# Optimization experiments

Measured on AMD Instinct MI355X. Metric: run time of the kernel, lower is better.

The kernel has to match this reference:

```python
import math
import jax, jax.numpy as jnp
import numpy as np

# ---- model dims ----
D = 4096          # hidden_size
N = 32            # num_attention_heads (== num_key_value_heads)
Q_LORA = 1536
KV_LORA = 512
QK_NOPE = 128
QK_ROPE = 64
QK_HEAD = QK_NOPE + QK_ROPE   # 192
V_HEAD = 128
EPS = 1e-6
T = 2048

# ---- yarn rope constants ----
ROPE_THETA = 10000.0
FACTOR = 40.0
ORIG_MAX = 4096
BETA_FAST = 32.0
BETA_SLOW = 1.0
MSCALE = 1.0
MSCALE_ALL_DIM = 1.0


def _yarn_get_mscale(scale, mscale):
    if scale <= 1.0:
        return 1.0
    return 0.1 * mscale * math.log(scale) + 1.0

# softmax scale: qk_head_dim^-0.5 * yarn_mscale^2 (rope_mscale_all_dim = 1.0)
YARN_MSCALE = _yarn_get_mscale(FACTOR, MSCALE_ALL_DIM)
SM_SCALE = QK_HEAD ** (-0.5) * YARN_MSCALE ** 2


def _yarn_cos_sin(positions):
    """DeepSeek yarn scaled rotary embeddings. positions: int [T]."""
    half = QK_ROPE // 2
    pow_ = np.arange(0, QK_ROPE, 2, dtype=np.float64) / QK_ROPE
    pos_freqs = ROPE_THETA ** pow_
    inv_extra = 1.0 / pos_freqs
    inv_inter = 1.0 / (FACTOR * pos_freqs)

    def corr_dim(n_rot):
        return (QK_ROPE * math.log(ORIG_MAX / (n_rot * 2 * math.pi))) / (2 * math.log(ROPE_THETA))

    low = max(math.floor(corr_dim(BETA_FAST)), 0)
    high = min(math.ceil(corr_dim(BETA_SLOW)), QK_ROPE - 1)
    ramp = np.clip((np.arange(half, dtype=np.float64) - low) / max(high - low, 1e-3), 0.0, 1.0)
    mask = 1.0 - ramp  # 1 where extrapolation
    inv_freq = inv_inter * (1.0 - mask) + inv_extra * mask
    inv_freq = jnp.asarray(inv_freq, jnp.float32)

    mscale_coef = _yarn_get_mscale(FACTOR, MSCALE) / _yarn_get_mscale(FACTOR, MSCALE_ALL_DIM)
    t = positions.astype(jnp.float32)
    freqs = t[:, None] * inv_freq[None, :]          # [T, half]
    return jnp.cos(freqs) * mscale_coef, jnp.sin(freqs) * mscale_coef


def _apply_rope(x_tnh, cos, sin):
    """Neox-style (split halves) rope. x: [T, N, QK_ROPE]; cos/sin: [T, half]."""
    half = QK_ROPE // 2
    x1, x2 = x_tnh[..., :half], x_tnh[..., half:]
    c, s = cos[:, None, :], sin[:, None, :]
    return jnp.concatenate([x1 * c - x2 * s, x1 * s + x2 * c], axis=-1)


def _rms_norm(x, scale, eps=EPS):
    var = jnp.mean(jnp.square(x), axis=-1, keepdims=True)
    return x * jax.lax.rsqrt(var + eps) * scale


def setup_inputs() -> dict:
    key = jax.random.key(0)
    ks = jax.random.split(key, 8)
    std = 0.02
    return {
        "x": jax.random.normal(ks[0], (T, D), jnp.float32),
        "positions": jnp.arange(T, dtype=jnp.int32),
        "w_q_down": jax.random.normal(ks[1], (D, Q_LORA), jnp.float32) * std,
        "q_norm_scale": jnp.ones((Q_LORA,), jnp.float32),
        "w_q_up": jax.random.normal(ks[2], (Q_LORA, N, QK_HEAD), jnp.float32) * std,
        "w_kv_down": jax.random.normal(ks[3], (D, KV_LORA + QK_ROPE), jnp.float32) * std,
        "kv_norm_scale": jnp.ones((KV_LORA,), jnp.float32),
        "w_kv_up": jax.random.normal(ks[4], (KV_LORA, N, QK_NOPE + V_HEAD), jnp.float32) * std,
        "w_o": jax.random.normal(ks[5], (N, V_HEAD, D), jnp.float32) * std,
    }


def reference(x, positions, w_q_down, q_norm_scale, w_q_up, w_kv_down,
              kv_norm_scale, w_kv_up, w_o):
    cos, sin = _yarn_cos_sin(positions)

    # ---- q projection (low rank) ----
    q_ta = _rms_norm(jnp.einsum('td,da->ta', x, w_q_down), q_norm_scale)
    q_tnh = jnp.einsum('ta,anh->tnh', q_ta, w_q_up)            # [T,N,192]
    q_rope = _apply_rope(q_tnh[..., QK_NOPE:], cos, sin)
    q_tnh = jnp.concatenate([q_tnh[..., :QK_NOPE], q_rope], axis=-1)

    # ---- kv projection (compressed latent) ----
    kv_sa = jnp.einsum('sd,da->sa', x, w_kv_down)              # [T, KV_LORA+64]
    k_rope = _apply_rope(kv_sa[:, None, KV_LORA:], cos, sin)   # [T,1,64]
    k_rope = jnp.broadcast_to(k_rope, (x.shape[0], N, QK_ROPE))
    kv_lat = _rms_norm(kv_sa[..., :KV_LORA], kv_norm_scale)
    kv_nope = jnp.einsum('sa,anh->snh', kv_lat, w_kv_up)       # [T,N,256]
    k_snh = jnp.concatenate([kv_nope[..., :QK_NOPE], k_rope], axis=-1)
    v_snh = kv_nope[..., QK_NOPE:]

    # ---- causal attention (prefill; padding to 128-multiple is a no-op) ----
    scores = jnp.einsum('tnh,snh->nts', q_tnh, k_snh) * SM_SCALE
    tpos = jnp.arange(x.shape[0])
    causal = tpos[:, None] >= tpos[None, :]
    scores = jnp.where(causal[None, :, :], scores, jnp.finfo(scores.dtype).min)
    probs = jax.nn.softmax(scores, axis=-1)
    out_tnh = jnp.einsum('nts,snh->tnh', probs, v_snh)

    # ---- output projection ----
    return jnp.einsum('tnh,nhd->td', out_tnh, w_o)
```

## Files before the change

### kernel.cpp

```cpp
#include <hip/hip_runtime.h>
#include <math.h>
#include <stdint.h>

#define T_    2048
#define D_    4096
#define NH_   32
#define QL_   1536
#define KVL_  512
#define ROPE_ 64
#define NOPE_ 128
#define HQK_  192
#define HV_   128
#define KVD_  576
#define NCAT_ 2112

typedef __bf16 bf16x8 __attribute__((ext_vector_type(8)));
typedef __bf16 bf16x4 __attribute__((ext_vector_type(4)));
typedef float f32x4 __attribute__((ext_vector_type(4)));

__device__ __forceinline__ void gload_lds16(const __bf16* g, __bf16* l) {
  __builtin_amdgcn_global_load_lds(
      (const __attribute__((address_space(1))) void*)g,
      (__attribute__((address_space(3))) void*)l, 16, 0, 0);
}

template <typename OutT>
__global__ __launch_bounds__(256, 3) void mfma_gemm_kernel(
    const __bf16* __restrict__ A, const __bf16* __restrict__ Bt,
    OutT* __restrict__ C, int M, int Ncols, int K) {
  __shared__ __bf16 As[128 * 64];
  __shared__ __bf16 Bs[128 * 64];
  const int tid = threadIdx.x;
  const int lane = tid & 63;
  const int w = tid >> 6;
  const int wm = w >> 1, wn = w & 1;
  const int lg = lane >> 4, lj = lane & 15;
  const int bm = blockIdx.y * 128;
  const int bn = blockIdx.x * 128;

  const __bf16* ga[4]; const __bf16* gb[4];
  int ldsoff[4];
  #pragma unroll
  for (int i = 0; i < 4; ++i) {
    int task = i * 256 + tid;
    int r = task >> 3, cl = task & 7;
    int cg = cl ^ (r & 7);
    ga[i] = A  + (size_t)(bm + r) * K + cg * 8;
    gb[i] = Bt + (size_t)(bn + r) * K + cg * 8;
    ldsoff[i] = (i * 256 + w * 64) * 8;
  }

  f32x4 acc[4][4];
  #pragma unroll
  for (int mi = 0; mi < 4; ++mi)
    #pragma unroll
    for (int ni = 0; ni < 4; ++ni) acc[mi][ni] = (f32x4){0.f, 0.f, 0.f, 0.f};

  for (int k0 = 0; k0 < K; k0 += 64) {
    __syncthreads();
    #pragma unroll
    for (int i = 0; i < 4; ++i) gload_lds16(ga[i] + k0, &As[ldsoff[i]]);
    #pragma unroll
    for (int i = 0; i < 4; ++i) gload_lds16(gb[i] + k0, &Bs[ldsoff[i]]);
    __syncthreads();
    #pragma unroll
    for (int kh = 0; kh < 2; ++kh) {
      bf16x8 af[4], bfr[4];
      #pragma unroll
      for (int i = 0; i < 4; ++i) {
        int ra = wm * 64 + i * 16 + lj;
        af[i] = *(const bf16x8*)&As[ra * 64 + ((((kh << 2) + lg) ^ (ra & 7)) << 3)];
      }
      #pragma unroll
      for (int i = 0; i < 4; ++i) {
        int rb = wn * 64 + i * 16 + lj;
        bfr[i] = *(const bf16x8*)&Bs[rb * 64 + ((((kh << 2) + lg) ^ (rb & 7)) << 3)];
      }
      #pragma unroll
      for (int mi = 0; mi < 4; ++mi)
        #pragma unroll
        for (int ni = 0; ni < 4; ++ni)
          acc[mi][ni] = __builtin_amdgcn_mfma_f32_16x16x32_bf16(af[mi], bfr[ni], acc[mi][ni], 0, 0, 0);
    }
  }

  #pragma unroll
  for (int mi = 0; mi < 4; ++mi) {
    #pragma unroll
    for (int r = 0; r < 4; ++r) {
      int row = bm + wm * 64 + mi * 16 + lg * 4 + r;
      #pragma unroll
      for (int ni = 0; ni < 4; ++ni) {
        int col = bn + wn * 64 + ni * 16 + lj;
        if (col < Ncols) C[(size_t)row * Ncols + col] = (OutT)acc[mi][ni][r];
      }
    }
  }
}

__global__ __launch_bounds__(256) void transpose_bf16_kernel(
    const float* __restrict__ B, __bf16* __restrict__ Bt, int K, int N) {
  __shared__ float tile[64][65];
  int n0 = blockIdx.x * 64, k0 = blockIdx.y * 64;
  int tid = threadIdx.x;
  int kr = tid >> 4, nc = (tid & 15) * 4;
  #pragma unroll
  for (int i = 0; i < 4; ++i) {
    int k = kr + i * 16;
    float4 v = make_float4(0.f, 0.f, 0.f, 0.f);
    if (n0 + nc < N) v = *(const float4*)(B + (size_t)(k0 + k) * N + n0 + nc);
    tile[k][nc + 0] = v.x; tile[k][nc + 1] = v.y;
    tile[k][nc + 2] = v.z; tile[k][nc + 3] = v.w;
  }
  __syncthreads();
  int nl = tid >> 4, k4 = (tid & 15) * 4;
  #pragma unroll
  for (int i = 0; i < 4; ++i) {
    int nn = nl + i * 16;
    bf16x4 o;
    o[0] = (__bf16)tile[k4 + 0][nn]; o[1] = (__bf16)tile[k4 + 1][nn];
    o[2] = (__bf16)tile[k4 + 2][nn]; o[3] = (__bf16)tile[k4 + 3][nn];
    *(bf16x4*)(Bt + (size_t)(n0 + nn) * K + k0 + k4) = o;
  }
}

__global__ __launch_bounds__(256) void conv_bf16_kernel(
    const float* __restrict__ in, __bf16* __restrict__ out, int n8) {
  int i = blockIdx.x * 256 + threadIdx.x;
  if (i >= n8) return;
  float4 a = *(const float4*)(in + (size_t)i * 8);
  float4 b = *(const float4*)(in + (size_t)i * 8 + 4);
  bf16x8 v;
  v[0] = (__bf16)a.x; v[1] = (__bf16)a.y; v[2] = (__bf16)a.z; v[3] = (__bf16)a.w;
  v[4] = (__bf16)b.x; v[5] = (__bf16)b.y; v[6] = (__bf16)b.z; v[7] = (__bf16)b.w;
  *(bf16x8*)(out + (size_t)i * 8) = v;
}

__global__ __launch_bounds__(256) void rmsnorm_bf16_kernel(
    const __bf16* __restrict__ in, __bf16* __restrict__ out,
    const float* __restrict__ scale, int len, int in_stride) {
  int row = blockIdx.x;
  const __bf16* x = in + (size_t)row * in_stride;
  __bf16* y = out + (size_t)row * len;
  float ss = 0.f;
  for (int i = threadIdx.x; i < len; i += 256) { float v = (float)x[i]; ss += v * v; }
  __shared__ float red[4];
  #pragma unroll
  for (int o = 32; o > 0; o >>= 1) ss += __shfl_down(ss, o, 64);
  int wid = threadIdx.x >> 6, lane = threadIdx.x & 63;
  if (lane == 0) red[wid] = ss;
  __syncthreads();
  if (threadIdx.x == 0) {
    float t = red[0] + red[1] + red[2] + red[3];
    red[0] = 1.0f / sqrtf(t / (float)len + 1e-6f);
  }
  __syncthreads();
  float r = red[0];
  for (int i = threadIdx.x; i < len; i += 256) y[i] = (__bf16)((float)x[i] * r * scale[i]);
}

struct InvFreq { float f[32]; };
__global__ __launch_bounds__(256) void rope_table_kernel(
    const int* __restrict__ pos, float* __restrict__ cosT, float* __restrict__ sinT,
    InvFreq invf) {
  int idx = blockIdx.x * 256 + threadIdx.x;
  if (idx >= T_ * 32) return;
  int t = idx >> 5, i = idx & 31;
  float fr = (float)pos[t] * invf.f[i];
  cosT[idx] = cosf(fr);
  sinT[idx] = sinf(fr);
}

__global__ __launch_bounds__(256) void rope_q_kernel(
    __bf16* __restrict__ q, const float* __restrict__ cosT, const float* __restrict__ sinT) {
  int idx = blockIdx.x * 256 + threadIdx.x;
  if (idx >= T_ * NH_ * 32) return;
  int i = idx & 31;
  int tn = idx >> 5;
  int t = tn >> 5;
  __bf16* b = q + (size_t)tn * HQK_ + NOPE_;
  float x1 = (float)b[i], x2 = (float)b[i + 32];
  float c = cosT[t * 32 + i], s = sinT[t * 32 + i];
  b[i]      = (__bf16)(x1 * c - x2 * s);
  b[i + 32] = (__bf16)(x1 * s + x2 * c);
}

__global__ __launch_bounds__(256) void rope_k_kernel(
    const __bf16* __restrict__ src, int stride, const float* __restrict__ cosT,
    const float* __restrict__ sinT, __bf16* __restrict__ k_rope) {
  int idx = blockIdx.x * 256 + threadIdx.x;
  if (idx >= T_ * 32) return;
  int t = idx >> 5, i = idx & 31;
  const __bf16* b = src + (size_t)t * stride;
  float x1 = (float)b[i], x2 = (float)b[i + 32];
  float c = cosT[idx], s = sinT[idx];
  k_rope[t * 64 + i]      = (__bf16)(x1 * c - x2 * s);
  k_rope[t * 64 + i + 32] = (__bf16)(x1 * s + x2 * c);
}

__global__ __launch_bounds__(256) void prep_vt_kernel(
    const __bf16* __restrict__ kv_nopeb, __bf16* __restrict__ Vt) {
  __shared__ __bf16 tile[64][136];
  int s0 = blockIdx.x * 64;
  int n = blockIdx.y;
  int tid = threadIdx.x;
  #pragma unroll
  for (int i = 0; i < 4; ++i) {
    int idx = tid + i * 256;
    int s = idx >> 4, c = idx & 15;
    bf16x8 v = *(const bf16x8*)(kv_nopeb + ((size_t)(s0 + s) * NH_ + n) * 256 + NOPE_ + c * 8);
    *(bf16x8*)&tile[s][c * 8] = v;
  }
  __syncthreads();
  #pragma unroll
  for (int i = 0; i < 8; ++i) {
    int idx = tid + i * 256;
    int h = idx >> 4, s4 = (idx & 15) * 4;
    bf16x4 v;
    v[0] = tile[s4 + 0][h]; v[1] = tile[s4 + 1][h];
    v[2] = tile[s4 + 2][h]; v[3] = tile[s4 + 3][h];
    *(bf16x4*)(Vt + ((size_t)n * HV_ + h) * T_ + s0 + s4) = v;
  }
}

__global__ __launch_bounds__(256, 2) void attn_mfma_kernel(
    const __bf16* __restrict__ q_tnh, const __bf16* __restrict__ kv_nopeb,
    const __bf16* __restrict__ k_rope, const __bf16* __restrict__ Vt,
    __bf16* __restrict__ attn_out, float sm_scale2) {
  __shared__ __bf16 KsL[2][24 * 64 * 8];
  __shared__ __bf16 Vs[8 * 128 * 8];
  __shared__ __bf16 Ps[4][32 * 64];
  const int tid = threadIdx.x;
  const int lane = tid & 63;
  const int w = tid >> 6;
  const int id = blockIdx.x;
  const int j = id >> 3;
  const int p = j >> 2;
  const int n = (id & 7) * 4 + (j & 3);
  const int lg = lane >> 4;
  const int lj = lane & 15;
  const int qtf0 = p, qtf1 = 31 - p;

  const __bf16* kptr[6]; size_t kstep[6]; int klds[6];
  #pragma unroll
  for (int i = 0; i < 6; ++i) {
    int task = i * 256 + tid;
    int c = task >> 6, s = task & 63;
    if (c < 16) { kptr[i] = kv_nopeb + ((size_t)s * NH_ + n) * 256 + c * 8; kstep[i] = (size_t)64 * NH_ * 256; }
    else        { kptr[i] = k_rope + (size_t)s * ROPE_ + (c - 16) * 8;      kstep[i] = (size_t)64 * ROPE_; }
    klds[i] = (i * 256 + w * 64) * 8;
  }
  const __bf16* vptr[4]; int vlds[4];
  #pragma unroll
  for (int i = 0; i < 4; ++i) {
    int task = i * 256 + tid;
    int c = task >> 7, h = task & 127;
    vptr[i] = Vt + ((size_t)n * HV_ + h) * T_ + c * 8;
    vlds[i] = (i * 256 + w * 64) * 8;
  }

  #define STAGE_K(bufIdx)                                                      \
    do {                                                                       \
      __bf16* kb_ = &KsL[bufIdx][0];                                           \
      _Pragma("unroll")                                                        \
      for (int i_ = 0; i_ < 6; ++i_) {                                         \
        gload_lds16(kptr[i_], kb_ + klds[i_]);                                 \
        kptr[i_] += kstep[i_];                                                 \
      }                                                                        \
    } while (0)
  #define STAGE_V()                                                            \
    do {                                                                       \
      _Pragma("unroll")                                                        \
      for (int i_ = 0; i_ < 4; ++i_) {                                         \
        gload_lds16(vptr[i_], &Vs[0] + vlds[i_]);                              \
        vptr[i_] += 64;                                                        \
      }                                                                        \
    } while (0)

  STAGE_K(0);

  bf16x8 qf[2][6];
  #pragma unroll
  for (int f = 0; f < 2; ++f) {
    int t = (f ? qtf1 : qtf0) * 64 + w * 16 + lj;
    const __bf16* qp = q_tnh + ((size_t)t * NH_ + n) * HQK_;
    #pragma unroll
    for (int kk = 0; kk < 6; ++kk) {
      bf16x8 raw = *(const bf16x8*)(qp + kk * 32 + lg * 8);
      bf16x8 v;
      #pragma unroll
      for (int i = 0; i < 8; ++i) v[i] = (__bf16)((float)raw[i] * sm_scale2);
      qf[f][kk] = v;
    }
  }

  f32x4 O[2][8];
  float m_r[2][4], l_r[2][4];
  #pragma unroll
  for (int f = 0; f < 2; ++f) {
    #pragma unroll
    for (int nb = 0; nb < 8; ++nb) O[f][nb] = (f32x4){0.f, 0.f, 0.f, 0.f};
    #pragma unroll
    for (int r = 0; r < 4; ++r) { m_r[f][r] = -1e30f; l_r[f][r] = 0.f; }
  }

  __syncthreads();

  const int nst = 32 - p;
  #pragma unroll 1
  for (int st = 0; st < nst; ++st) {
    const int s0 = st * 64;
    const int cur = st & 1;
    if (st + 1 < nst) STAGE_K(cur ^ 1);
    STAGE_V();
    const __bf16* kb = &KsL[cur][0];
    const bool act0 = (st <= qtf0);

    #pragma unroll
    for (int f = 0; f < 2; ++f) {
      if (f == 0 && !act0) continue;
      const int qt = f ? qtf1 : qtf0;
      const int rowbase = qt * 64 + w * 16;
      f32x4 S[4];
      __builtin_amdgcn_s_setprio(1);
      #pragma unroll
      for (int sb = 0; sb < 4; ++sb) {
        f32x4 acc = (f32x4){0.f, 0.f, 0.f, 0.f};
        int srow = sb * 16 + lj;
        #pragma unroll
        for (int kk = 0; kk < 6; ++kk) {
          int c = kk * 4 + lg;
          bf16x8 b = *(const bf16x8*)&kb[(c * 64 + srow) * 8];
          acc = __builtin_amdgcn_mfma_f32_16x16x32_bf16(qf[f][kk], b, acc, 0, 0, 0);
        }
        S[sb] = acc;
      }
      __builtin_amdgcn_s_setprio(0);
      if (st == qt) {
        #pragma unroll
        for (int sb = 0; sb < 4; ++sb)
          #pragma unroll
          for (int r = 0; r < 4; ++r) {
            int row = rowbase + lg * 4 + r;
            int col = s0 + sb * 16 + lj;
            if (col > row) S[sb][r] = -1e30f;
          }
      }
      float mx[4];
      #pragma unroll
      for (int r = 0; r < 4; ++r) {
        float m2 = fmaxf(fmaxf(S[0][r], S[1][r]), fmaxf(S[2][r], S[3][r]));
        m2 = fmaxf(m2, __shfl_xor(m2, 1));
        m2 = fmaxf(m2, __shfl_xor(m2, 2));
        m2 = fmaxf(m2, __shfl_xor(m2, 4));
        m2 = fmaxf(m2, __shfl_xor(m2, 8));
        mx[r] = m2;
      }
      int need = (mx[0] > m_r[f][0]) | (mx[1] > m_r[f][1]) |
                 (mx[2] > m_r[f][2]) | (mx[3] > m_r[f][3]);
      if (__any(need)) {
        #pragma unroll
        for (int r = 0; r < 4; ++r) {
          float mnew = fmaxf(m_r[f][r], mx[r]);
          float corr = __builtin_amdgcn_exp2f(m_r[f][r] - mnew);
          m_r[f][r] = mnew;
          l_r[f][r] *= corr;
          #pragma unroll
          for (int nb = 0; nb < 8; ++nb) O[f][nb][r] = O[f][nb][r] * corr;
        }
      }
      #pragma unroll
      for (int r = 0; r < 4; ++r) {
        float psum = 0.f;
        #pragma unroll
        for (int sb = 0; sb < 4; ++sb) {
          float pp = __builtin_amdgcn_exp2f(S[sb][r] - m_r[f][r]);
          S[sb][r] = pp;
          psum += pp;
        }
        l_r[f][r] += psum;
      }
      #pragma unroll
      for (int sb = 0; sb < 4; ++sb) {
        int sl = sb * 16 + lj;
        int c = sl >> 3;
        #pragma unroll
        for (int r = 0; r < 4; ++r) {
          int rw = lg * 4 + r;
          Ps[w][(f * 16 + rw) * 64 + ((c ^ (rw & 7)) << 3) + (sl & 7)] = (__bf16)S[sb][r];
        }
      }
    }
    __syncthreads();
    __builtin_amdgcn_s_setprio(1);
    #pragma unroll
    for (int f = 0; f < 2; ++f) {
      if (f == 0 && !act0) continue;
      #pragma unroll
      for (int kk = 0; kk < 2; ++kk) {
        int ca = kk * 4 + lg;
        bf16x8 pa = *(const bf16x8*)&Ps[w][(f * 16 + lj) * 64 + ((ca ^ (lj & 7)) << 3)];
        #pragma unroll
        for (int nb = 0; nb < 8; ++nb) {
          int h = nb * 16 + lj;
          bf16x8 bv = *(const bf16x8*)&Vs[(ca * 128 + h) * 8];
          O[f][nb] = __builtin_amdgcn_mfma_f32_16x16x32_bf16(pa, bv, O[f][nb], 0, 0, 0);
        }
      }
    }
    __builtin_amdgcn_s_setprio(0);
    __syncthreads();
  }

  #pragma unroll
  for (int f = 0; f < 2; ++f) {
    const int qt = f ? qtf1 : qtf0;
    #pragma unroll
    for (int r = 0; r < 4; ++r) {
      float lsum = l_r[f][r];
      lsum += __shfl_xor(lsum, 1);
      lsum += __shfl_xor(lsum, 2);
      lsum += __shfl_xor(lsum, 4);
      lsum += __shfl_xor(lsum, 8);
      float inv = 1.0f / lsum;
      int t = qt * 64 + w * 16 + lg * 4 + r;
      __bf16* dst = attn_out + ((size_t)t * NH_ + n) * HV_;
      #pragma unroll
      for (int nb = 0; nb < 8; ++nb) dst[nb * 16 + lj] = (__bf16)(O[f][nb][r] * inv);
    }
  }
  #undef STAGE_K
  #undef STAGE_V
}

static void compute_inv_freq(float* out) {
  const double theta = 10000.0, factor = 40.0;
  const double PI = 3.14159265358979323846;
  const int rot = ROPE_;
  double low_d  = rot * log(4096.0 / (32.0 * 2.0 * PI)) / (2.0 * log(theta));
  double high_d = rot * log(4096.0 / ( 1.0 * 2.0 * PI)) / (2.0 * log(theta));
  double low = floor(low_d);  if (low < 0) low = 0;
  double high = ceil(high_d); if (high > rot - 1) high = rot - 1;
  for (int i = 0; i < 32; ++i) {
    double pf = pow(theta, (2.0 * i) / (double)rot);
    double inv_extra = 1.0 / pf;
    double inv_inter = 1.0 / (factor * pf);
    double ramp = ((double)i - low) / fmax(high - low, 0.001);
    ramp = fmin(fmax(ramp, 0.0), 1.0);
    double mask = 1.0 - ramp;
    out[i] = (float)(inv_inter * (1.0 - mask) + inv_extra * mask);
  }
}

extern "C" void kernel_launch(void* const* d_in, const int* in_sizes, int n_in,
                              void* d_out, int out_size, void* d_ws, size_t ws_size,
                              hipStream_t stream) {
  const float* x            = (const float*)d_in[0];
  const int*   positions    = (const int*)d_in[1];
  const float* w_q_down     = (const float*)d_in[2];
  const float* q_norm_scale = (const float*)d_in[3];
  const float* w_q_up       = (const float*)d_in[4];
  const float* w_kv_down    = (const float*)d_in[5];
  const float* kv_norm_scale= (const float*)d_in[6];
  const float* w_kv_up      = (const float*)d_in[7];
  const float* w_o          = (const float*)d_in[8];
  float* out = (float*)d_out;

  float* ws = (float*)d_ws;
  float*  cosT     = ws;
  float*  sinT     = ws + 65536;
  __bf16* catb     = (__bf16*)(ws + 131072);
  __bf16* xb       = (__bf16*)(ws + 4456448);
  __bf16* Bt_cat   = (__bf16*)(ws + 8650752);
  __bf16* Bt_qu    = (__bf16*)(ws + 13107200);
  __bf16* Bt_kvu   = (__bf16*)(ws + 17825792);
  __bf16* q_tab    = (__bf16*)(ws + 19922944);
  __bf16* kv_latb  = (__bf16*)(ws + 21495808);
  __bf16* k_ropeb  = (__bf16*)(ws + 22020096);
  __bf16* q_tnhb   = (__bf16*)(ws + 22085632);
  __bf16* kv_nopeb = (__bf16*)(ws + 28377088);
  __bf16* Vt       = (__bf16*)(ws + 13107200);
  __bf16* attn_ob  = (__bf16*)(ws + 17825792);
  __bf16* Bt_o     = (__bf16*)(ws + 4456448);
  (void)ws_size; (void)n_in; (void)in_sizes; (void)out_size;

  InvFreq invf;
  compute_inv_freq(invf.f);
  double ym = 0.1 * log(40.0) + 1.0;
  float sm_scale2 = (float)((ym * ym / sqrt((double)HQK_)) * 1.44269504088896340736);

  rope_table_kernel<<<(T_ * 32 + 255) / 256, 256, 0, stream>>>(positions, cosT, sinT, invf);
  conv_bf16_kernel<<<T_ * D_ / 8 / 256, 256, 0, stream>>>(x, xb, T_ * D_ / 8);
  transpose_bf16_kernel<<<dim3(QL_ / 64, D_ / 64), 256, 0, stream>>>(w_q_down, Bt_cat, D_, QL_);
  transpose_bf16_kernel<<<dim3(KVD_ / 64, D_ / 64), 256, 0, stream>>>(w_kv_down, Bt_cat + (size_t)QL_ * D_, D_, KVD_);
  transpose_bf16_kernel<<<dim3(NH_ * HQK_ / 64, QL_ / 64), 256, 0, stream>>>(w_q_up, Bt_qu, QL_, NH_ * HQK_);
  transpose_bf16_kernel<<<dim3(NH_ * 256 / 64, KVL_ / 64), 256, 0, stream>>>(w_kv_up, Bt_kvu, KVL_, NH_ * 256);

  mfma_gemm_kernel<__bf16><<<dim3((NCAT_ + 127) / 128, T_ / 128), 256, 0, stream>>>(xb, Bt_cat, catb, T_, NCAT_, D_);

  rmsnorm_bf16_kernel<<<T_, 256, 0, stream>>>(catb, q_tab, q_norm_scale, QL_, NCAT_);
  mfma_gemm_kernel<__bf16><<<dim3(NH_ * HQK_ / 128, T_ / 128), 256, 0, stream>>>(q_tab, Bt_qu, q_tnhb, T_, NH_ * HQK_, QL_);
  rope_q_kernel<<<(T_ * NH_ * 32 + 255) / 256, 256, 0, stream>>>(q_tnhb, cosT, sinT);

  rmsnorm_bf16_kernel<<<T_, 256, 0, stream>>>(catb + QL_, kv_latb, kv_norm_scale, KVL_, NCAT_);
  rope_k_kernel<<<(T_ * 32 + 255) / 256, 256, 0, stream>>>(catb + QL_ + KVL_, NCAT_, cosT, sinT, k_ropeb);
  mfma_gemm_kernel<__bf16><<<dim3(NH_ * 256 / 128, T_ / 128), 256, 0, stream>>>(kv_latb, Bt_kvu, kv_nopeb, T_, NH_ * 256, KVL_);

  prep_vt_kernel<<<dim3(T_ / 64, NH_), 256, 0, stream>>>(kv_nopeb, Vt);
  attn_mfma_kernel<<<512, 256, 0, stream>>>(q_tnhb, kv_nopeb, k_ropeb, Vt, attn_ob, sm_scale2);

  transpose_bf16_kernel<<<dim3(D_ / 64, NH_ * HV_ / 64), 256, 0, stream>>>(w_o, Bt_o, NH_ * HV_, D_);
  mfma_gemm_kernel<float><<<dim3(D_ / 128, T_ / 128), 256, 0, stream>>>(attn_ob, Bt_o, out, T_, D_, NH_ * HV_);
}
```

Baseline: 412.3 us.

## Fuse V transpose into kv-up GEMM epilogue and use BK=128 for down projection

The kv-up projection GEMM now computes the V half of each head with operands swapped, so it writes V already transposed into the Vt buffer. This removes the separate prep_vt transpose kernel and its extra read and write of V. The fused down projection uses a new GEMM variant with a 128-wide K tile, halving the number of K iterations and barriers, at the cost of 64KB of LDS per block. The transposed stores are less coalesced than the normal epilogue.

```diff
diff --git a/kernel.cpp b/kernel.cpp
--- a/kernel.cpp
+++ b/kernel.cpp
@@ -98,6 +98,179 @@
   }
 }
 
+template <typename OutT>
+__global__ __launch_bounds__(256, 2) void mfma_gemm_bk128_kernel(
+    const __bf16* __restrict__ A, const __bf16* __restrict__ Bt,
+    OutT* __restrict__ C, int M, int Ncols, int K) {
+  __shared__ __bf16 As[128 * 128];
+  __shared__ __bf16 Bs[128 * 128];
+  const int tid = threadIdx.x;
+  const int lane = tid & 63;
+  const int w = tid >> 6;
+  const int wm = w >> 1, wn = w & 1;
+  const int lg = lane >> 4, lj = lane & 15;
+  const int bm = blockIdx.y * 128;
+  const int bn = blockIdx.x * 128;
+
+  const __bf16* ga[8]; const __bf16* gb[8];
+  int ldsoff[8];
+  #pragma unroll
+  for (int i = 0; i < 8; ++i) {
+    int task = i * 256 + tid;
+    int r = task >> 4, cl = task & 15;
+    int cg = (cl & 8) | ((cl & 7) ^ (r & 7));
+    ga[i] = A  + (size_t)(bm + r) * K + cg * 8;
+    gb[i] = Bt + (size_t)(bn + r) * K + cg * 8;
+    ldsoff[i] = (i * 256 + w * 64) * 8;
+  }
+
+  f32x4 acc[4][4];
+  #pragma unroll
+  for (int mi = 0; mi < 4; ++mi)
+    #pragma unroll
+    for (int ni = 0; ni < 4; ++ni) acc[mi][ni] = (f32x4){0.f, 0.f, 0.f, 0.f};
+
+  for (int k0 = 0; k0 < K; k0 += 128) {
+    __syncthreads();
+    #pragma unroll
+    for (int i = 0; i < 8; ++i) gload_lds16(ga[i] + k0, &As[ldsoff[i]]);
+    #pragma unroll
+    for (int i = 0; i < 8; ++i) gload_lds16(gb[i] + k0, &Bs[ldsoff[i]]);
+    __syncthreads();
+    #pragma unroll
+    for (int kh = 0; kh < 4; ++kh) {
+      bf16x8 af[4], bfr[4];
+      #pragma unroll
+      for (int i = 0; i < 4; ++i) {
+        int ra = wm * 64 + i * 16 + lj;
+        int kc = (kh << 2) + lg;
+        int slot = (kc & 8) | ((kc & 7) ^ (ra & 7));
+        af[i] = *(const bf16x8*)&As[ra * 128 + (slot << 3)];
+      }
+      #pragma unroll
+      for (int i = 0; i < 4; ++i) {
+        int rb = wn * 64 + i * 16 + lj;
+        int kc = (kh << 2) + lg;
+        int slot = (kc & 8) | ((kc & 7) ^ (rb & 7));
+        bfr[i] = *(const bf16x8*)&Bs[rb * 128 + (slot << 3)];
+      }
+      #pragma unroll
+      for (int mi = 0; mi < 4; ++mi)
+        #pragma unroll
+        for (int ni = 0; ni < 4; ++ni)
+          acc[mi][ni] = __builtin_amdgcn_mfma_f32_16x16x32_bf16(af[mi], bfr[ni], acc[mi][ni], 0, 0, 0);
+    }
+  }
+
+  #pragma unroll
+  for (int mi = 0; mi < 4; ++mi) {
+    #pragma unroll
+    for (int r = 0; r < 4; ++r) {
+      int row = bm + wm * 64 + mi * 16 + lg * 4 + r;
+      #pragma unroll
+      for (int ni = 0; ni < 4; ++ni) {
+        int col = bn + wn * 64 + ni * 16 + lj;
+        if (col < Ncols) C[(size_t)row * Ncols + col] = (OutT)acc[mi][ni][r];
+      }
+    }
+  }
+}
+
+__global__ __launch_bounds__(256, 3) void kvup_gemm_kernel(
+    const __bf16* __restrict__ A ,
+    const __bf16* __restrict__ Bt ,
+    __bf16* __restrict__ kv_nopeb ,
+    __bf16* __restrict__ Vt ) {
+  __shared__ __bf16 As[128 * 64];
+  __shared__ __bf16 Bs[128 * 64];
+  const int tid = threadIdx.x;
+  const int lane = tid & 63;
+  const int w = tid >> 6;
+  const int wm = w >> 1, wn = w & 1;
+  const int lg = lane >> 4, lj = lane & 15;
+  const int bm = blockIdx.y * 128;
+  const int bn = blockIdx.x * 128;
+  const int n = blockIdx.x >> 1;
+  const bool vhalf = (blockIdx.x & 1) != 0;
+  const int K = KVL_;
+
+  const __bf16* ga[4]; const __bf16* gb[4];
+  int ldsoff[4];
+  #pragma unroll
+  for (int i = 0; i < 4; ++i) {
+    int task = i * 256 + tid;
+    int r = task >> 3, cl = task & 7;
+    int cg = cl ^ (r & 7);
+    ga[i] = A  + (size_t)(bm + r) * K + cg * 8;
+    gb[i] = Bt + (size_t)(bn + r) * K + cg * 8;
+    ldsoff[i] = (i * 256 + w * 64) * 8;
+  }
+
+  const __bf16* RowT = vhalf ? &Bs[0] : &As[0];
+  const __bf16* ColT = vhalf ? &As[0] : &Bs[0];
+
+  f32x4 acc[4][4];
+  #pragma unroll
+  for (int mi = 0; mi < 4; ++mi)
+    #pragma unroll
+    for (int ni = 0; ni < 4; ++ni) acc[mi][ni] = (f32x4){0.f, 0.f, 0.f, 0.f};
+
+  for (int k0 = 0; k0 < K; k0 += 64) {
+    __syncthreads();
+    #pragma unroll
+    for (int i = 0; i < 4; ++i) gload_lds16(ga[i] + k0, &As[ldsoff[i]]);
+    #pragma unroll
+    for (int i = 0; i < 4; ++i) gload_lds16(gb[i] + k0, &Bs[ldsoff[i]]);
+    __syncthreads();
+    #pragma unroll
+    for (int kh = 0; kh < 2; ++kh) {
+      bf16x8 af[4], bfr[4];
+      #pragma unroll
+      for (int i = 0; i < 4; ++i) {
+        int ra = wm * 64 + i * 16 + lj;
+        af[i] = *(const bf16x8*)&RowT[ra * 64 + ((((kh << 2) + lg) ^ (ra & 7)) << 3)];
+      }
+      #pragma unroll
+      for (int i = 0; i < 4; ++i) {
+        int rb = wn * 64 + i * 16 + lj;
+        bfr[i] = *(const bf16x8*)&ColT[rb * 64 + ((((kh << 2) + lg) ^ (rb & 7)) << 3)];
+      }
+      #pragma unroll
+      for (int mi = 0; mi < 4; ++mi)
+        #pragma unroll
+        for (int ni = 0; ni < 4; ++ni)
+          acc[mi][ni] = __builtin_amdgcn_mfma_f32_16x16x32_bf16(af[mi], bfr[ni], acc[mi][ni], 0, 0, 0);
+    }
+  }
+
+  if (!vhalf) {
+    #pragma unroll
+    for (int mi = 0; mi < 4; ++mi)
+      #pragma unroll
+      for (int r = 0; r < 4; ++r) {
+        int s = bm + wm * 64 + mi * 16 + lg * 4 + r;
+        #pragma unroll
+        for (int ni = 0; ni < 4; ++ni) {
+          int c = wn * 64 + ni * 16 + lj;
+          kv_nopeb[((size_t)s * NH_ + n) * 256 + c] = (__bf16)acc[mi][ni][r];
+        }
+      }
+  } else {
+    #pragma unroll
+    for (int mi = 0; mi < 4; ++mi)
+      #pragma unroll
+      for (int r = 0; r < 4; ++r) {
+        int h = wm * 64 + mi * 16 + lg * 4 + r;
+        __bf16* dst = Vt + ((size_t)n * HV_ + h) * T_ + bm;
+        #pragma unroll
+        for (int ni = 0; ni < 4; ++ni) {
+          int s = wn * 64 + ni * 16 + lj;
+          dst[s] = (__bf16)acc[mi][ni][r];
+        }
+      }
+  }
+}
+
 __global__ __launch_bounds__(256) void transpose_bf16_kernel(
     const float* __restrict__ B, __bf16* __restrict__ Bt, int K, int N) {
   __shared__ float tile[64][65];
@@ -196,31 +369,6 @@
   float c = cosT[idx], s = sinT[idx];
   k_rope[t * 64 + i]      = (__bf16)(x1 * c - x2 * s);
   k_rope[t * 64 + i + 32] = (__bf16)(x1 * s + x2 * c);
-}
-
-__global__ __launch_bounds__(256) void prep_vt_kernel(
-    const __bf16* __restrict__ kv_nopeb, __bf16* __restrict__ Vt) {
-  __shared__ __bf16 tile[64][136];
-  int s0 = blockIdx.x * 64;
-  int n = blockIdx.y;
-  int tid = threadIdx.x;
-  #pragma unroll
-  for (int i = 0; i < 4; ++i) {
-    int idx = tid + i * 256;
-    int s = idx >> 4, c = idx & 15;
-    bf16x8 v = *(const bf16x8*)(kv_nopeb + ((size_t)(s0 + s) * NH_ + n) * 256 + NOPE_ + c * 8);
-    *(bf16x8*)&tile[s][c * 8] = v;
-  }
-  __syncthreads();
-  #pragma unroll
-  for (int i = 0; i < 8; ++i) {
-    int idx = tid + i * 256;
-    int h = idx >> 4, s4 = (idx & 15) * 4;
-    bf16x4 v;
-    v[0] = tile[s4 + 0][h]; v[1] = tile[s4 + 1][h];
-    v[2] = tile[s4 + 2][h]; v[3] = tile[s4 + 3][h];
-    *(bf16x4*)(Vt + ((size_t)n * HV_ + h) * T_ + s0 + s4) = v;
-  }
 }
 
 __global__ __launch_bounds__(256, 2) void attn_mfma_kernel(
@@ -496,7 +644,7 @@
   transpose_bf16_kernel<<<dim3(NH_ * HQK_ / 64, QL_ / 64), 256, 0, stream>>>(w_q_up, Bt_qu, QL_, NH_ * HQK_);
   transpose_bf16_kernel<<<dim3(NH_ * 256 / 64, KVL_ / 64), 256, 0, stream>>>(w_kv_up, Bt_kvu, KVL_, NH_ * 256);
 
-  mfma_gemm_kernel<__bf16><<<dim3((NCAT_ + 127) / 128, T_ / 128), 256, 0, stream>>>(xb, Bt_cat, catb, T_, NCAT_, D_);
+  mfma_gemm_bk128_kernel<__bf16><<<dim3((NCAT_ + 127) / 128, T_ / 128), 256, 0, stream>>>(xb, Bt_cat, catb, T_, NCAT_, D_);
 
   rmsnorm_bf16_kernel<<<T_, 256, 0, stream>>>(catb, q_tab, q_norm_scale, QL_, NCAT_);
   mfma_gemm_kernel<__bf16><<<dim3(NH_ * HQK_ / 128, T_ / 128), 256, 0, stream>>>(q_tab, Bt_qu, q_tnhb, T_, NH_ * HQK_, QL_);
@@ -504,9 +652,8 @@
 
   rmsnorm_bf16_kernel<<<T_, 256, 0, stream>>>(catb + QL_, kv_latb, kv_norm_scale, KVL_, NCAT_);
   rope_k_kernel<<<(T_ * 32 + 255) / 256, 256, 0, stream>>>(catb + QL_ + KVL_, NCAT_, cosT, sinT, k_ropeb);
-  mfma_gemm_kernel<__bf16><<<dim3(NH_ * 256 / 128, T_ / 128), 256, 0, stream>>>(kv_latb, Bt_kvu, kv_nopeb, T_, NH_ * 256, KVL_);
-
-  prep_vt_kernel<<<dim3(T_ / 64, NH_), 256, 0, stream>>>(kv_nopeb, Vt);
+  kvup_gemm_kernel<<<dim3(NH_ * 2, T_ / 128), 256, 0, stream>>>(kv_latb, Bt_kvu, kv_nopeb, Vt);
+
   attn_mfma_kernel<<<512, 256, 0, stream>>>(q_tnhb, kv_nopeb, k_ropeb, Vt, attn_ob, sm_scale2);
 
   transpose_bf16_kernel<<<dim3(D_ / 64, NH_ * HV_ / 64), 256, 0, stream>>>(w_o, Bt_o, NH_ * HV_, D_);
```

Result: faster. 389.9 us (-5.4%).
